# Kernel optimization log

Measured on AMD Instinct MI355X. Metric: run time of the kernel, lower is better.

The kernel has to match this reference:

```python
import jax, jax.numpy as jnp
import numpy as np

HID, HEADS, LAYERS = 64, 4, 2
D = HID // HEADS
NU, NE, NV = 30000, 60000, 1000
N_NODES = (NU, NE, NV)
OFFS = (0, NU, NU + NE, NU + NE + NV)
N_TOTAL = NU + NE + NV
# (src_type, dst_type, n_edges); node types: user=0, event=1, venue=2. Order matches module.edge_types.
EDGE_DEFS = (
    (0, 0, 150000),  # friend
    (0, 1, 120000), (0, 1, 60000), (0, 1, 40000), (0, 1, 30000), (0, 1, 50000),  # view/like/save/intent/attend
    (1, 0, 120000), (1, 0, 60000), (1, 0, 40000), (1, 0, 30000), (1, 0, 50000),  # rev_*
    (1, 2, 60000),  # hosted_at
    (2, 1, 60000),  # hosts
)
EDGE_NAMES = ('ei_friend', 'ei_view', 'ei_like', 'ei_save', 'ei_intent', 'ei_attend',
              'ei_rev_view', 'ei_rev_like', 'ei_rev_save', 'ei_rev_intent', 'ei_rev_attend',
              'ei_hosted_at', 'ei_hosts')


def _l2norm(x):
    return x / jnp.maximum(jnp.linalg.norm(x, axis=-1, keepdims=True), 1e-12)


def _hgt_layer(h, edges, Wkqv, bkqv, Wk, Wv, p_rel, Wout, bout, skip):
    # h: list of per-node-type features [N_t, HID]. Fused K/Q/V projection per node type.
    kqv = [h[t] @ Wkqv[t] + bkqv[t] for t in range(3)]  # [N_t, 3*HID]
    k = [a[:, :HID].reshape(-1, HEADS, D) for a in kqv]
    q = [a[:, HID:2 * HID].reshape(-1, HEADS, D) for a in kqv]
    v = [a[:, 2 * HID:].reshape(-1, HEADS, D) for a in kqv]
    scale = 1.0 / np.sqrt(D).astype(np.float32)
    scores, msgs, dsts = [], [], []
    for e, (s, d, _) in enumerate(EDGE_DEFS):
        src_idx, dst_idx = edges[e][0], edges[e][1]
        # per-(edge_type, head) DxD relation transforms (PyG k_rel / v_rel)
        ke = jnp.einsum('nhd,hde->nhe', k[s], Wk[e])[src_idx]  # [E,H,D]
        ve = jnp.einsum('nhd,hde->nhe', v[s], Wv[e])[src_idx]  # [E,H,D]
        qi = q[d][dst_idx]                                      # [E,H,D]
        scores.append((qi * ke).sum(-1) * p_rel[e] * scale)     # [E,H]
        msgs.append(ve)
        dsts.append(dst_idx + OFFS[d])
    sc = jnp.concatenate(scores)   # [E_tot, H]
    ms = jnp.concatenate(msgs)     # [E_tot, H, D]
    dst = jnp.concatenate(dsts)    # [E_tot] global destination ids
    # destination-grouped softmax across all edge types jointly
    smax = jax.lax.stop_gradient(jax.ops.segment_max(sc, dst, num_segments=N_TOTAL))
    ex = jnp.exp(sc - smax[dst])
    den = jax.ops.segment_sum(ex, dst, num_segments=N_TOTAL)
    alpha = ex / den[dst]
    agg = jax.ops.segment_sum(alpha[:, :, None] * ms, dst, num_segments=N_TOTAL).reshape(N_TOTAL, HID)
    out = []
    for t in range(3):
        o = agg[OFFS[t]:OFFS[t + 1]]
        a = jax.nn.gelu(o, approximate=False) @ Wout[t] + bout[t]
        g = jax.nn.sigmoid(skip[t])  # learnable skip gate
        out.append(g * a + (1.0 - g) * h[t])
    return out


def _forward(x_user, x_event, x_venue, W_user, b_user, W_event, b_event, W_venue, b_venue,
             emb_user, emb_event, emb_venue, Wkqv, bkqv, Wk, Wv, p_rel, Wout, bout, skip,
             ids_user, ids_event, ids_venue, edges):
    h = [x_user @ W_user + b_user + emb_user[ids_user],
         x_event @ W_event + b_event + emb_event[ids_event],
         x_venue @ W_venue + b_venue + emb_venue[ids_venue]]
    for l in range(LAYERS):
        h = _hgt_layer(h, edges, Wkqv[l], bkqv[l], Wk[l], Wv[l], p_rel[l], Wout[l], bout[l], skip[l])
        h = [jax.nn.relu(x) for x in h]  # dropout is identity in eval mode
    return tuple(_l2norm(x) for x in h)


def setup_inputs() -> dict:
    key = jax.random.key(0)
    ks = iter(jax.random.split(key, 64))
    s = 0.05
    inp = {
        'x_user': jax.random.normal(next(ks), (NU, 32), jnp.float32),
        'x_event': jax.random.normal(next(ks), (NE, 32), jnp.float32),
        'x_venue': jax.random.normal(next(ks), (NV, 16), jnp.float32),
        'W_user': jax.random.normal(next(ks), (32, HID), jnp.float32) * s,
        'b_user': jnp.zeros((HID,), jnp.float32),
        'W_event': jax.random.normal(next(ks), (32, HID), jnp.float32) * s,
        'b_event': jnp.zeros((HID,), jnp.float32),
        'W_venue': jax.random.normal(next(ks), (16, HID), jnp.float32) * s,
        'b_venue': jnp.zeros((HID,), jnp.float32),
        'emb_user': jax.random.normal(next(ks), (NU, HID), jnp.float32) * s,
        'emb_event': jax.random.normal(next(ks), (NE, HID), jnp.float32) * s,
        'emb_venue': jax.random.normal(next(ks), (NV, HID), jnp.float32) * s,
        'Wkqv': jax.random.normal(next(ks), (LAYERS, 3, HID, 3 * HID), jnp.float32) * s,
        'bkqv': jnp.zeros((LAYERS, 3, 3 * HID), jnp.float32),
        'Wk': jax.random.normal(next(ks), (LAYERS, 13, HEADS, D, D), jnp.float32) * 0.2,
        'Wv': jax.random.normal(next(ks), (LAYERS, 13, HEADS, D, D), jnp.float32) * 0.2,
        'p_rel': jnp.ones((LAYERS, 13, HEADS), jnp.float32),
        'Wout': jax.random.normal(next(ks), (LAYERS, 3, HID, HID), jnp.float32) * s,
        'bout': jnp.zeros((LAYERS, 3, HID), jnp.float32),
        'skip': jnp.ones((LAYERS, 3), jnp.float32),
        'ids_user': jnp.arange(NU, dtype=jnp.int32),
        'ids_event': jnp.arange(NE, dtype=jnp.int32),
        'ids_venue': jnp.arange(NV, dtype=jnp.int32),
    }
    for name, (st, dt, n) in zip(EDGE_NAMES, EDGE_DEFS):
        src = jax.random.randint(next(ks), (n,), 0, N_NODES[st], dtype=jnp.int32)
        dst = jax.random.randint(next(ks), (n,), 0, N_NODES[dt], dtype=jnp.int32)
        inp[name] = jnp.stack([src, dst])
    return inp


def reference(x_user, x_event, x_venue, W_user, b_user, W_event, b_event, W_venue, b_venue,
              emb_user, emb_event, emb_venue, Wkqv, bkqv, Wk, Wv, p_rel, Wout, bout, skip,
              ids_user, ids_event, ids_venue,
              ei_friend, ei_view, ei_like, ei_save, ei_intent, ei_attend,
              ei_rev_view, ei_rev_like, ei_rev_save, ei_rev_intent, ei_rev_attend,
              ei_hosted_at, ei_hosts):
    edges = (ei_friend, ei_view, ei_like, ei_save, ei_intent, ei_attend,
             ei_rev_view, ei_rev_like, ei_rev_save, ei_rev_intent, ei_rev_attend,
             ei_hosted_at, ei_hosts)
    return _forward(x_user, x_event, x_venue, W_user, b_user, W_event, b_event, W_venue, b_venue,
                    emb_user, emb_event, emb_venue, Wkqv, bkqv, Wk, Wv, p_rel, Wout, bout, skip,
                    ids_user, ids_event, ids_venue, edges)
```

## Files before the change

kernel.cpp:

```cpp
#include <hip/hip_runtime.h>
#include <hip/hip_fp16.h>
#include <math.h>

#define HID   64
#define HEADS 4
#define DH    16
#define NU    30000
#define NE_   60000
#define NV    1000
#define NTOT  91000
#define ETOT  870000
#define NSLOT 541000
#define LAYERS 2

__device__ const int d_EOFF[14] = {0,150000,270000,330000,370000,400000,450000,
                                   570000,630000,670000,700000,750000,810000,870000};
__device__ const int d_ECNT[13] = {150000,120000,60000,40000,30000,50000,
                                   120000,60000,40000,30000,50000,60000,60000};
__device__ const int d_EST[13]  = {0,0,0,0,0,0,1,1,1,1,1,1,2};
__device__ const int d_EDT[13]  = {0,1,1,1,1,1,0,0,0,0,0,2,1};
__device__ const int d_NOFF[3]  = {0, NU, NU + NE_};
__device__ const int d_EBASE[13] = {0,30000,60000,90000,120000,150000,
                                    180000,240000,300000,360000,420000,480000,540000};

struct EdgePtrs { const int* p[13]; };

__device__ __forceinline__ int node_type(int n) {
    return (n >= NU) + (n >= NU + NE_);
}

__device__ __forceinline__ float dot16(const float4 a0, const float4 a1,
                                       const float4 a2, const float4 a3,
                                       const float* w) {
    return a0.x*w[0] + a0.y*w[1] + a0.z*w[2] + a0.w*w[3]
         + a1.x*w[4] + a1.y*w[5] + a1.z*w[6] + a1.w*w[7]
         + a2.x*w[8] + a2.y*w[9] + a2.z*w[10]+ a2.w*w[11]
         + a3.x*w[12]+ a3.y*w[13]+ a3.z*w[14]+ a3.w*w[15];
}

__global__ void k_init(const float* __restrict__ xu, const float* __restrict__ xe,
                       const float* __restrict__ xv,
                       const float* __restrict__ Wu, const float* __restrict__ bu,
                       const float* __restrict__ We, const float* __restrict__ be,
                       const float* __restrict__ Wv_, const float* __restrict__ bv,
                       const float* __restrict__ embu, const float* __restrict__ embe,
                       const float* __restrict__ embv,
                       const int* __restrict__ idu, const int* __restrict__ ide,
                       const int* __restrict__ idv,
                       float* __restrict__ h) {
    int gid = blockIdx.x * blockDim.x + threadIdx.x;
    if (gid >= NTOT * HID) return;
    int node = gid >> 6, j = gid & 63;
    const float *x, *W, *b, *emb; const int* ids; int in_dim, n;
    if (node < NU)            { n = node;           x = xu; W = Wu;  b = bu; emb = embu; ids = idu; in_dim = 32; }
    else if (node < NU + NE_) { n = node - NU;      x = xe; W = We;  b = be; emb = embe; ids = ide; in_dim = 32; }
    else                      { n = node - NU - NE_;x = xv; W = Wv_; b = bv; emb = embv; ids = idv; in_dim = 16; }
    float acc = b[j] + emb[(size_t)ids[n] * HID + j];
    for (int i = 0; i < in_dim; i++) acc += x[(size_t)n * in_dim + i] * W[i * HID + j];
    h[gid] = acc;
}

__global__ void k_cnt(EdgePtrs ep, int* __restrict__ cnt) {
    int eidx = blockIdx.x * blockDim.x + threadIdx.x;
    if (eidx >= ETOT) return;
    int e = 0;
    #pragma unroll
    for (int i = 1; i < 13; i++) e += (eidx >= d_EOFF[i]);
    int li = eidx - d_EOFF[e];
    int dst = ep.p[e][d_ECNT[e] + li];
    atomicAdd(&cnt[d_NOFF[d_EDT[e]] + dst], 1);
}

__global__ void k_scan_a(const int* __restrict__ cnt, int* __restrict__ partial) {
    __shared__ int s[256];
    int i = blockIdx.x * 256 + threadIdx.x;
    s[threadIdx.x] = (i < NTOT) ? cnt[i] : 0;
    __syncthreads();
    for (int off = 128; off > 0; off >>= 1) {
        if (threadIdx.x < off) s[threadIdx.x] += s[threadIdx.x + off];
        __syncthreads();
    }
    if (threadIdx.x == 0) partial[blockIdx.x] = s[0];
}

__global__ void k_scan_b(int* __restrict__ partial, int nblk) {
    __shared__ int s[512];
    int t = threadIdx.x;
    s[t] = (t < nblk) ? partial[t] : 0;
    __syncthreads();
    for (int off = 1; off < 512; off <<= 1) {
        int v = (t >= off) ? s[t - off] : 0;
        __syncthreads();
        s[t] += v;
        __syncthreads();
    }
    if (t < nblk) partial[t] = t ? s[t - 1] : 0;
}

__global__ void k_scan_c(const int* __restrict__ cnt, const int* __restrict__ partial,
                         int* __restrict__ row_ptr) {
    __shared__ int s[256];
    int i = blockIdx.x * 256 + threadIdx.x, t = threadIdx.x;
    int v = (i < NTOT) ? cnt[i] : 0;
    s[t] = v;
    __syncthreads();
    for (int off = 1; off < 256; off <<= 1) {
        int u = (t >= off) ? s[t - off] : 0;
        __syncthreads();
        s[t] += u;
        __syncthreads();
    }
    if (i < NTOT) row_ptr[i] = s[t] - v + partial[blockIdx.x];
    if (i == NTOT - 1) row_ptr[NTOT] = s[t] + partial[blockIdx.x];
}

__global__ void k_fill(EdgePtrs ep, const int* __restrict__ row_ptr,
                       int* __restrict__ cursor, int* __restrict__ csr) {
    int eidx = blockIdx.x * blockDim.x + threadIdx.x;
    if (eidx >= ETOT) return;
    int e = 0;
    #pragma unroll
    for (int i = 1; i < 13; i++) e += (eidx >= d_EOFF[i]);
    int li = eidx - d_EOFF[e];
    const int* base = ep.p[e];
    int src = base[li], dst = base[d_ECNT[e] + li];
    int dg = d_NOFF[d_EDT[e]] + dst;
    int pos = atomicAdd(&cursor[dg], 1);
    csr[row_ptr[dg] + pos] = d_EBASE[e] + src;
}

__global__ __launch_bounds__(192, 4)
void k_kqvt(const float* __restrict__ h, const float* __restrict__ Wkqv,
            const float* __restrict__ bkqv, const float* __restrict__ Wk,
            const float* __restrict__ Wv, const float* __restrict__ prel,
            float* __restrict__ qagg, __half2* __restrict__ kvt, int layer) {
    int n0 = blockIdx.x * 16;
    int t = node_type(n0);
    __shared__ float kq[16][192];
    int j = threadIdx.x;
    const float* W = Wkqv + (size_t)(layer * 3 + t) * HID * 192;
    float wreg[64];
    #pragma unroll
    for (int i = 0; i < 64; i++) wreg[i] = W[i * 192 + j];
    float b = bkqv[(layer * 3 + t) * 192 + j];
    float acc[16];
    #pragma unroll
    for (int n = 0; n < 16; n++) acc[n] = b;
    const float* hb = h + (size_t)n0 * 64;
    #pragma unroll
    for (int ic = 0; ic < 16; ic++) {
        #pragma unroll
        for (int n = 0; n < 16; n++) {
            float4 hv = *(const float4*)(hb + n * 64 + ic * 4);
            acc[n] += hv.x * wreg[4*ic]   + hv.y * wreg[4*ic+1]
                    + hv.z * wreg[4*ic+2] + hv.w * wreg[4*ic+3];
        }
    }
    #pragma unroll
    for (int n = 0; n < 16; n++) kq[n][j] = acc[n];
    if (j >= 64 && j < 128) {
        #pragma unroll
        for (int n = 0; n < 16; n++)
            if (n0 + n < NTOT) qagg[(size_t)(n0 + n) * 64 + (j - 64)] = acc[n];
    }
    __syncthreads();
    int wave = j >> 6, lane = j & 63;
    int hh = lane >> 4, xo = lane & 15;
    int ne = (t == 2) ? 1 : 6;
    int e0 = (t == 0) ? 0 : (t == 1) ? 6 : 12;
    int eA = e0 + wave, eB = e0 + wave + 3;
    bool vA = wave < ne, vB = wave + 3 < ne;
    int nt = n0 - d_NOFF[t];
    float wkA[16], wvA[16], wkB[16], wvB[16];
    int sbA = 0, sbB = 0;
    if (vA) {
        const float* Wkp = Wk + (((size_t)layer * 13 + eA) * 4 + hh) * 256 + xo;
        const float* Wvp = Wv + (((size_t)layer * 13 + eA) * 4 + hh) * 256 + xo;
        float pr = prel[(layer * 13 + eA) * 4 + hh] * 0.25f;
        #pragma unroll
        for (int d = 0; d < 16; d++) { wkA[d] = Wkp[d * 16] * pr; wvA[d] = Wvp[d * 16]; }
        sbA = d_EBASE[eA] + nt;
    }
    if (vB) {
        const float* Wkp = Wk + (((size_t)layer * 13 + eB) * 4 + hh) * 256 + xo;
        const float* Wvp = Wv + (((size_t)layer * 13 + eB) * 4 + hh) * 256 + xo;
        float pr = prel[(layer * 13 + eB) * 4 + hh] * 0.25f;
        #pragma unroll
        for (int d = 0; d < 16; d++) { wkB[d] = Wkp[d * 16] * pr; wvB[d] = Wvp[d * 16]; }
        sbB = d_EBASE[eB] + nt;
    }
    #pragma unroll
    for (int n = 0; n < 16; n++) {
        bool ok = (n0 + n) < NTOT;
        const float* kr = &kq[n][hh * 16];
        const float* vr = &kq[n][128 + hh * 16];
        float4 k0 = *(const float4*)(kr);
        float4 k1 = *(const float4*)(kr + 4);
        float4 k2 = *(const float4*)(kr + 8);
        float4 k3 = *(const float4*)(kr + 12);
        float4 v0 = *(const float4*)(vr);
        float4 v1 = *(const float4*)(vr + 4);
        float4 v2 = *(const float4*)(vr + 8);
        float4 v3 = *(const float4*)(vr + 12);
        if (vA & ok) {
            float kt = dot16(k0, k1, k2, k3, wkA);
            float vt = dot16(v0, v1, v2, v3, wvA);
            kvt[(size_t)(sbA + n) * 64 + lane] = __float22half2_rn(make_float2(kt, vt));
        }
        if (vB & ok) {
            float kt = dot16(k0, k1, k2, k3, wkB);
            float vt = dot16(v0, v1, v2, v3, wvB);
            kvt[(size_t)(sbB + n) * 64 + lane] = __float22half2_rn(make_float2(kt, vt));
        }
    }
}

__device__ __forceinline__ float row_sum16(float x) {
    int v;
    v = __builtin_amdgcn_update_dpp(0, __float_as_int(x), 0xB1, 0xF, 0xF, true);
    x += __int_as_float(v);
    v = __builtin_amdgcn_update_dpp(0, __float_as_int(x), 0x4E, 0xF, 0xF, true);
    x += __int_as_float(v);
    v = __builtin_amdgcn_update_dpp(0, __float_as_int(x), 0x141, 0xF, 0xF, true);
    x += __int_as_float(v);
    v = __builtin_amdgcn_update_dpp(0, __float_as_int(x), 0x140, 0xF, 0xF, true);
    x += __int_as_float(v);
    return x;
}

__device__ __forceinline__ void osm_step(float s, float vv,
                                         float& m, float& l, float& acc) {
    float d = s - m;
    float t = __expf(-fabsf(d));
    bool pos = d > 0.f;
    m = fmaxf(m, s);
    float sc = pos ? t : 1.f;
    float es = pos ? 1.f : t;
    l   = l * sc + es;
    acc = acc * sc + es * vv;
}

__global__ __launch_bounds__(512)
void k_gather(float* __restrict__ qagg, const __half2* __restrict__ kvt,
              const int* __restrict__ row_ptr, const int* __restrict__ csr) {
    int wave = threadIdx.x >> 6, lane = threadIdx.x & 63;
    int node = blockIdx.x * 8 + wave;
    if (node >= NTOT) return;
    float q = qagg[(size_t)node * 64 + lane];
    int beg = row_ptr[node], end = row_ptr[node + 1];
    float m0 = -1e30f, l0 = 0.f, a0 = 0.f;
    float m1 = -1e30f, l1 = 0.f, a1 = 0.f;
    for (int base = beg; base < end; base += 64) {
        int n = end - base; if (n > 64) n = 64;
        int ent = csr[base + ((lane < n) ? lane : 0)];
        for (int c = 0; c < n; c += 8) {
            int cn = n - c; if (cn > 8) cn = 8;
            __half2 f[8];
            #pragma unroll
            for (int k = 0; k < 8; k++) {
                int idx = c + ((k < cn) ? k : 0);
                int sl = __shfl(ent, idx, 64);
                f[k] = kvt[(size_t)sl * 64 + lane];
            }
            float s8[8];
            #pragma unroll
            for (int k = 0; k < 8; k++) {
                if (k >= cn) break;
                s8[k] = row_sum16(q * __low2float(f[k]));
            }
            #pragma unroll
            for (int k = 0; k < 8; k += 2) {
                if (k < cn)     osm_step(s8[k],   __high2float(f[k]),   m0, l0, a0);
                if (k + 1 < cn) osm_step(s8[k+1], __high2float(f[k+1]), m1, l1, a1);
            }
        }
    }
    float M   = fmaxf(m0, m1);
    float e0  = __expf(m0 - M), e1 = __expf(m1 - M);
    float l   = l0 * e0 + l1 * e1;
    float acc = a0 * e0 + a1 * e1;
    qagg[(size_t)node * 64 + lane] = (l > 0.f) ? acc / l : 0.f;
}

__global__ __launch_bounds__(256)
void k_out(const float* __restrict__ agg, const float* __restrict__ Wout,
           const float* __restrict__ bout, const float* __restrict__ skip,
           float* __restrict__ h, float* __restrict__ out, int layer, int last) {
    int b = blockIdx.x; int t, n0, lim;
    if (b < 938)       { t = 0; n0 = b * 32;                 lim = NU; }
    else if (b < 2813) { t = 1; n0 = NU + (b - 938) * 32;    lim = NU + NE_; }
    else               { t = 2; n0 = NU + NE_ + (b - 2813) * 32; lim = NTOT; }
    int nn = min(32, lim - n0);
    __shared__ float gs[32][64];
    for (int i = threadIdx.x; i < nn * 64; i += 256) {
        float o = agg[(size_t)n0 * 64 + i];
        gs[i >> 6][i & 63] = 0.5f * o * (1.f + erff(o * 0.70710678118654752f));
    }
    __syncthreads();
    int j = threadIdx.x & 63, g = threadIdx.x >> 6;
    const float* W = Wout + (size_t)(layer * 3 + t) * HID * HID;
    float bb = bout[(layer * 3 + t) * HID + j];
    float acc[8];
    #pragma unroll
    for (int n = 0; n < 8; n++) acc[n] = bb;
    for (int i = 0; i < 64; i++) {
        float w = W[i * 64 + j];
        #pragma unroll
        for (int n = 0; n < 8; n++) acc[n] += gs[g * 8 + n][i] * w;
    }
    float gk = 1.f / (1.f + __expf(-skip[layer * 3 + t]));
    #pragma unroll
    for (int n = 0; n < 8; n++) {
        int node = n0 + g * 8 + n;
        if (node >= lim) continue;
        float r = gk * acc[n] + (1.f - gk) * h[(size_t)node * 64 + j];
        r = fmaxf(r, 0.f);
        if (!last) {
            h[(size_t)node * 64 + j] = r;
        } else {
            float ss = r * r;
            ss += __shfl_xor(ss, 1, 64);  ss += __shfl_xor(ss, 2, 64);
            ss += __shfl_xor(ss, 4, 64);  ss += __shfl_xor(ss, 8, 64);
            ss += __shfl_xor(ss, 16, 64); ss += __shfl_xor(ss, 32, 64);
            float nrm = fmaxf(sqrtf(ss), 1e-12f);
            out[(size_t)node * 64 + j] = r / nrm;
        }
    }
}

extern "C" void kernel_launch(void* const* d_in, const int* in_sizes, int n_in,
                              void* d_out, int out_size, void* d_ws, size_t ws_size,
                              hipStream_t stream) {
    const float* xu   = (const float*)d_in[0];
    const float* xe   = (const float*)d_in[1];
    const float* xv   = (const float*)d_in[2];
    const float* Wu   = (const float*)d_in[3];
    const float* bu   = (const float*)d_in[4];
    const float* We   = (const float*)d_in[5];
    const float* be   = (const float*)d_in[6];
    const float* Wv_  = (const float*)d_in[7];
    const float* bv   = (const float*)d_in[8];
    const float* embu = (const float*)d_in[9];
    const float* embe = (const float*)d_in[10];
    const float* embv = (const float*)d_in[11];
    const float* Wkqv = (const float*)d_in[12];
    const float* bkqv = (const float*)d_in[13];
    const float* Wk   = (const float*)d_in[14];
    const float* Wv   = (const float*)d_in[15];
    const float* prel = (const float*)d_in[16];
    const float* Wout = (const float*)d_in[17];
    const float* bout = (const float*)d_in[18];
    const float* skip = (const float*)d_in[19];
    const int*   idu  = (const int*)d_in[20];
    const int*   ide  = (const int*)d_in[21];
    const int*   idv  = (const int*)d_in[22];
    EdgePtrs ep;
    for (int e = 0; e < 13; e++) ep.p[e] = (const int*)d_in[23 + e];

    float* ws  = (float*)d_ws;
    float* h      = ws;
    float* qagg   = h    + (size_t)NTOT * HID;
    __half2* kvt  = (__half2*)(qagg + (size_t)NTOT * HID);
    int* cnt     = (int*)(kvt + (size_t)NSLOT * HID);
    int* cursor  = cnt + NTOT;
    int* row_ptr = cursor + NTOT;
    int* partial = row_ptr + NTOT + 1;
    int* csr     = partial + 512;

    k_init<<<(NTOT * HID + 255) / 256, 256, 0, stream>>>(
        xu, xe, xv, Wu, bu, We, be, Wv_, bv, embu, embe, embv, idu, ide, idv, h);

    hipMemsetAsync(cnt, 0, (size_t)2 * NTOT * 4, stream);
    int nblk = (NTOT + 255) / 256;
    k_cnt<<<(ETOT + 255) / 256, 256, 0, stream>>>(ep, cnt);
    k_scan_a<<<nblk, 256, 0, stream>>>(cnt, partial);
    k_scan_b<<<1, 512, 0, stream>>>(partial, nblk);
    k_scan_c<<<nblk, 256, 0, stream>>>(cnt, partial, row_ptr);
    k_fill<<<(ETOT + 255) / 256, 256, 0, stream>>>(ep, row_ptr, cursor, csr);

    for (int l = 0; l < LAYERS; l++) {
        k_kqvt<<<(NTOT + 15) / 16, 192, 0, stream>>>(h, Wkqv, bkqv, Wk, Wv, prel,
                                                     qagg, kvt, l);
        k_gather<<<(NTOT + 7) / 8, 512, 0, stream>>>(qagg, kvt, row_ptr, csr);
        k_out<<<2845, 256, 0, stream>>>(qagg, Wout, bout, skip, h,
                                        (float*)d_out, l, l == LAYERS - 1);
    }
}
```

Before: 718.0 us.

## Split fused KQV/relation-transform kernel into projection and per-edge-type transform kernels

New measurement: 1.187 ms. 65.4% more time.

```diff
diff --git a/kernel.cpp b/kernel.cpp
--- a/kernel.cpp
+++ b/kernel.cpp
@@ -22,20 +22,22 @@
 __device__ const int d_NOFF[3]  = {0, NU, NU + NE_};
 __device__ const int d_EBASE[13] = {0,30000,60000,90000,120000,150000,
                                     180000,240000,300000,360000,420000,480000,540000};
+__device__ const int d_NSRC[13] = {30000,30000,30000,30000,30000,30000,
+                                   60000,60000,60000,60000,60000,60000,1000};
+__device__ const int d_TOFF[13] = {0,469,938,1407,1876,2345,2814,
+                                   3752,4690,5628,6566,7504,8442};
+#define NWAVE_KVT 8458
 
 struct EdgePtrs { const int* p[13]; };
+
+typedef float f32x2 __attribute__((ext_vector_type(2)));
+
+__device__ __forceinline__ void pk_fma(f32x2& acc, f32x2 a, f32x2 b) {
+    asm("v_pk_fma_f32 %0, %1, %2, %0" : "+v"(acc) : "v"(a), "v"(b));
+}
 
 __device__ __forceinline__ int node_type(int n) {
     return (n >= NU) + (n >= NU + NE_);
-}
-
-__device__ __forceinline__ float dot16(const float4 a0, const float4 a1,
-                                       const float4 a2, const float4 a3,
-                                       const float* w) {
-    return a0.x*w[0] + a0.y*w[1] + a0.z*w[2] + a0.w*w[3]
-         + a1.x*w[4] + a1.y*w[5] + a1.z*w[6] + a1.w*w[7]
-         + a2.x*w[8] + a2.y*w[9] + a2.z*w[10]+ a2.w*w[11]
-         + a3.x*w[12]+ a3.y*w[13]+ a3.z*w[14]+ a3.w*w[15];
 }
 
 __global__ void k_init(const float* __restrict__ xu, const float* __restrict__ xe,
@@ -130,88 +132,107 @@
 }
 
 __global__ __launch_bounds__(192, 4)
-void k_kqvt(const float* __restrict__ h, const float* __restrict__ Wkqv,
-            const float* __restrict__ bkqv, const float* __restrict__ Wk,
-            const float* __restrict__ Wv, const float* __restrict__ prel,
-            float* __restrict__ qagg, __half2* __restrict__ kvt, int layer) {
+void k_kqv(const float* __restrict__ h, const float* __restrict__ Wkqv,
+           const float* __restrict__ bkqv,
+           float* __restrict__ qagg, float* __restrict__ kv, int layer) {
     int n0 = blockIdx.x * 16;
     int t = node_type(n0);
-    __shared__ float kq[16][192];
     int j = threadIdx.x;
     const float* W = Wkqv + (size_t)(layer * 3 + t) * HID * 192;
-    float wreg[64];
-    #pragma unroll
-    for (int i = 0; i < 64; i++) wreg[i] = W[i * 192 + j];
+    float acc[16];
     float b = bkqv[(layer * 3 + t) * 192 + j];
-    float acc[16];
     #pragma unroll
     for (int n = 0; n < 16; n++) acc[n] = b;
     const float* hb = h + (size_t)n0 * 64;
     #pragma unroll
     for (int ic = 0; ic < 16; ic++) {
+        float w0 = W[(4 * ic + 0) * 192 + j];
+        float w1 = W[(4 * ic + 1) * 192 + j];
+        float w2 = W[(4 * ic + 2) * 192 + j];
+        float w3 = W[(4 * ic + 3) * 192 + j];
         #pragma unroll
         for (int n = 0; n < 16; n++) {
             float4 hv = *(const float4*)(hb + n * 64 + ic * 4);
-            acc[n] += hv.x * wreg[4*ic]   + hv.y * wreg[4*ic+1]
-                    + hv.z * wreg[4*ic+2] + hv.w * wreg[4*ic+3];
+            acc[n] += hv.x * w0 + hv.y * w1 + hv.z * w2 + hv.w * w3;
         }
     }
     #pragma unroll
-    for (int n = 0; n < 16; n++) kq[n][j] = acc[n];
-    if (j >= 64 && j < 128) {
-        #pragma unroll
-        for (int n = 0; n < 16; n++)
-            if (n0 + n < NTOT) qagg[(size_t)(n0 + n) * 64 + (j - 64)] = acc[n];
-    }
-    __syncthreads();
-    int wave = j >> 6, lane = j & 63;
-    int hh = lane >> 4, xo = lane & 15;
-    int ne = (t == 2) ? 1 : 6;
-    int e0 = (t == 0) ? 0 : (t == 1) ? 6 : 12;
-    int eA = e0 + wave, eB = e0 + wave + 3;
-    bool vA = wave < ne, vB = wave + 3 < ne;
-    int nt = n0 - d_NOFF[t];
-    float wkA[16], wvA[16], wkB[16], wvB[16];
-    int sbA = 0, sbB = 0;
-    if (vA) {
-        const float* Wkp = Wk + (((size_t)layer * 13 + eA) * 4 + hh) * 256 + xo;
-        const float* Wvp = Wv + (((size_t)layer * 13 + eA) * 4 + hh) * 256 + xo;
-        float pr = prel[(layer * 13 + eA) * 4 + hh] * 0.25f;
-        #pragma unroll
-        for (int d = 0; d < 16; d++) { wkA[d] = Wkp[d * 16] * pr; wvA[d] = Wvp[d * 16]; }
-        sbA = d_EBASE[eA] + nt;
-    }
-    if (vB) {
-        const float* Wkp = Wk + (((size_t)layer * 13 + eB) * 4 + hh) * 256 + xo;
-        const float* Wvp = Wv + (((size_t)layer * 13 + eB) * 4 + hh) * 256 + xo;
-        float pr = prel[(layer * 13 + eB) * 4 + hh] * 0.25f;
-        #pragma unroll
-        for (int d = 0; d < 16; d++) { wkB[d] = Wkp[d * 16] * pr; wvB[d] = Wvp[d * 16]; }
-        sbB = d_EBASE[eB] + nt;
-    }
-    #pragma unroll
     for (int n = 0; n < 16; n++) {
-        bool ok = (n0 + n) < NTOT;
-        const float* kr = &kq[n][hh * 16];
-        const float* vr = &kq[n][128 + hh * 16];
-        float4 k0 = *(const float4*)(kr);
-        float4 k1 = *(const float4*)(kr + 4);
-        float4 k2 = *(const float4*)(kr + 8);
-        float4 k3 = *(const float4*)(kr + 12);
-        float4 v0 = *(const float4*)(vr);
-        float4 v1 = *(const float4*)(vr + 4);
-        float4 v2 = *(const float4*)(vr + 8);
-        float4 v3 = *(const float4*)(vr + 12);
-        if (vA & ok) {
-            float kt = dot16(k0, k1, k2, k3, wkA);
-            float vt = dot16(v0, v1, v2, v3, wvA);
-            kvt[(size_t)(sbA + n) * 64 + lane] = __float22half2_rn(make_float2(kt, vt));
-        }
-        if (vB & ok) {
-            float kt = dot16(k0, k1, k2, k3, wkB);
-            float vt = dot16(v0, v1, v2, v3, wvB);
-            kvt[(size_t)(sbB + n) * 64 + lane] = __float22half2_rn(make_float2(kt, vt));
-        }
+        int node = n0 + n;
+        if (node >= NTOT) break;
+        if (j < 64)       kv[(size_t)node * 128 + j] = acc[n];
+        else if (j < 128) qagg[(size_t)node * 64 + (j - 64)] = acc[n];
+        else              kv[(size_t)node * 128 + 64 + (j - 128)] = acc[n];
+    }
+}
+
+__global__ __launch_bounds__(256, 4)
+void k_kvt(const float* __restrict__ kv, const float* __restrict__ Wk,
+           const float* __restrict__ Wv, const float* __restrict__ prel,
+           __half2* __restrict__ kvt, int layer) {
+    int w = blockIdx.x * 4 + (threadIdx.x >> 6);
+    if (w >= NWAVE_KVT) return;
+    int e = 0;
+    #pragma unroll
+    for (int i = 1; i < 13; i++) e += (w >= d_TOFF[i]);
+    int ti = w - d_TOFF[e];
+    int n0 = ti * 64;
+    int nn = min(64, d_NSRC[e] - n0);
+    int lane = threadIdx.x & 63, hh = lane >> 4, xo = lane & 15;
+
+    const float* Wkp = Wk + (((size_t)layer * 13 + e) * 4 + hh) * 256 + xo;
+    const float* Wvp = Wv + (((size_t)layer * 13 + e) * 4 + hh) * 256 + xo;
+    float pr = prel[(layer * 13 + e) * 4 + hh] * 0.25f;
+    f32x2 wk2[8], wv2[8];
+    #pragma unroll
+    for (int p = 0; p < 8; p++) {
+        wk2[p].x = Wkp[(2 * p)     * 16] * pr;
+        wk2[p].y = Wkp[(2 * p + 1) * 16] * pr;
+        wv2[p].x = Wvp[(2 * p)     * 16];
+        wv2[p].y = Wvp[(2 * p + 1) * 16];
+    }
+
+    const float* kvb = kv + (size_t)(d_NOFF[d_EST[e]] + n0) * 128 + hh * 16;
+    __half2* outp = kvt + (size_t)(d_EBASE[e] + n0) * 64 + lane;
+
+    auto body = [&](int n) {
+        const float* kr = kvb + (size_t)n * 128;
+        float4 ka = ((const float4*)kr)[0];
+        float4 kb = ((const float4*)kr)[1];
+        float4 kc = ((const float4*)kr)[2];
+        float4 kd = ((const float4*)kr)[3];
+        float4 va = ((const float4*)(kr + 64))[0];
+        float4 vb = ((const float4*)(kr + 64))[1];
+        float4 vc = ((const float4*)(kr + 64))[2];
+        float4 vd = ((const float4*)(kr + 64))[3];
+        f32x2 ak; ak.x = 0.f; ak.y = 0.f;
+        f32x2 av; av.x = 0.f; av.y = 0.f;
+        f32x2 p0;
+        p0.x = ka.x; p0.y = ka.y; pk_fma(ak, p0, wk2[0]);
+        p0.x = ka.z; p0.y = ka.w; pk_fma(ak, p0, wk2[1]);
+        p0.x = kb.x; p0.y = kb.y; pk_fma(ak, p0, wk2[2]);
+        p0.x = kb.z; p0.y = kb.w; pk_fma(ak, p0, wk2[3]);
+        p0.x = kc.x; p0.y = kc.y; pk_fma(ak, p0, wk2[4]);
+        p0.x = kc.z; p0.y = kc.w; pk_fma(ak, p0, wk2[5]);
+        p0.x = kd.x; p0.y = kd.y; pk_fma(ak, p0, wk2[6]);
+        p0.x = kd.z; p0.y = kd.w; pk_fma(ak, p0, wk2[7]);
+        p0.x = va.x; p0.y = va.y; pk_fma(av, p0, wv2[0]);
+        p0.x = va.z; p0.y = va.w; pk_fma(av, p0, wv2[1]);
+        p0.x = vb.x; p0.y = vb.y; pk_fma(av, p0, wv2[2]);
+        p0.x = vb.z; p0.y = vb.w; pk_fma(av, p0, wv2[3]);
+        p0.x = vc.x; p0.y = vc.y; pk_fma(av, p0, wv2[4]);
+        p0.x = vc.z; p0.y = vc.w; pk_fma(av, p0, wv2[5]);
+        p0.x = vd.x; p0.y = vd.y; pk_fma(av, p0, wv2[6]);
+        p0.x = vd.z; p0.y = vd.w; pk_fma(av, p0, wv2[7]);
+        float kt = ak.x + ak.y;
+        float vt = av.x + av.y;
+        outp[(size_t)n * 64] = __float22half2_rn(make_float2(kt, vt));
+    };
+    if (nn == 64) {
+        #pragma unroll 4
+        for (int n = 0; n < 64; n++) body(n);
+    } else {
+        for (int n = 0; n < nn; n++) body(n);
     }
 }
 
@@ -360,7 +381,8 @@
     float* ws  = (float*)d_ws;
     float* h      = ws;
     float* qagg   = h    + (size_t)NTOT * HID;
-    __half2* kvt  = (__half2*)(qagg + (size_t)NTOT * HID);
+    float* kv     = qagg + (size_t)NTOT * HID;
+    __half2* kvt  = (__half2*)(kv + (size_t)NTOT * 128);
     int* cnt     = (int*)(kvt + (size_t)NSLOT * HID);
     int* cursor  = cnt + NTOT;
     int* row_ptr = cursor + NTOT;
@@ -379,8 +401,8 @@
     k_fill<<<(ETOT + 255) / 256, 256, 0, stream>>>(ep, row_ptr, cursor, csr);
 
     for (int l = 0; l < LAYERS; l++) {
-        k_kqvt<<<(NTOT + 15) / 16, 192, 0, stream>>>(h, Wkqv, bkqv, Wk, Wv, prel,
-                                                     qagg, kvt, l);
+        k_kqv<<<(NTOT + 15) / 16, 192, 0, stream>>>(h, Wkqv, bkqv, qagg, kv, l);
+        k_kvt<<<(NWAVE_KVT + 3) / 4, 256, 0, stream>>>(kv, Wk, Wv, prel, kvt, l);
         k_gather<<<(NTOT + 7) / 8, 512, 0, stream>>>(qagg, kvt, row_ptr, csr);
         k_out<<<2845, 256, 0, stream>>>(qagg, Wout, bout, skip, h,
                                         (float*)d_out, l, l == LAYERS - 1);
```
